# Performance work log

Measured on AMD Instinct MI355X. Metric: run time of the kernel, lower is better.

The kernel has to match this reference:

```python
import jax, jax.numpy as jnp
import numpy as np

D = 128      # d_model
H = 4        # n_heads
DH = D // H  # 32 head dim
TD = int(DH * 0.25)  # 8 time dims per head
T_DIM = TD * H       # 32 model-level time dims (MinkowskiLayerNorm t_dim)
EPS = 1e-5


def _ln(v, g, b):
    mu = jnp.mean(v, axis=-1, keepdims=True)
    var = jnp.mean(jnp.square(v - mu), axis=-1, keepdims=True)
    return (v - mu) * jax.lax.rsqrt(var + EPS) * g + b


def _minkowski_ln(x, gt, bt, gs, bs):
    # Normalize time-like and space-like coordinate blocks separately.
    return jnp.concatenate([_ln(x[..., :T_DIM], gt, bt), _ln(x[..., T_DIM:], gs, bs)], axis=-1)


def _lorentz_attn(x, Wq, bq, Wk, bk, Wv, bv, Wo, bo):
    B, S, _ = x.shape
    split = lambda y: y.reshape(B, S, H, DH).transpose(0, 2, 1, 3)  # [B,H,S,DH]
    q = split(x @ Wq + bq)
    k = split(x @ Wk + bk)
    v = split(x @ Wv + bv)
    # Minkowski metric signature (-,...,-,+,...,+): first TD dims of each head are time-like.
    eta = jnp.concatenate([-jnp.ones((TD,), x.dtype), jnp.ones((DH - TD,), x.dtype)])
    logits = jnp.einsum('bhqd,bhkd->bhqk', q * eta, k) / np.float32(np.sqrt(DH))
    w = jax.nn.softmax(logits, axis=-1)  # [B,H,S,S]
    o = jnp.einsum('bhqk,bhkd->bhqd', w, v).transpose(0, 2, 1, 3).reshape(B, S, D)
    return o @ Wo + bo


def setup_inputs() -> dict:
    key = jax.random.key(0)
    ks = jax.random.split(key, 8)
    s = 0.02
    inp = {
        'x': jax.random.normal(ks[0], (8, 2048, D), jnp.float32),
        'Wq': jax.random.normal(ks[1], (D, D), jnp.float32) * s,
        'bq': jnp.zeros((D,), jnp.float32),
        'Wk': jax.random.normal(ks[2], (D, D), jnp.float32) * s,
        'bk': jnp.zeros((D,), jnp.float32),
        'Wv': jax.random.normal(ks[3], (D, D), jnp.float32) * s,
        'bv': jnp.zeros((D,), jnp.float32),
        'Wo': jax.random.normal(ks[4], (D, D), jnp.float32) * s,
        'bo': jnp.zeros((D,), jnp.float32),
        'g1t': jnp.ones((T_DIM,), jnp.float32), 'b1t': jnp.zeros((T_DIM,), jnp.float32),
        'g1s': jnp.ones((D - T_DIM,), jnp.float32), 'b1s': jnp.zeros((D - T_DIM,), jnp.float32),
        'W1': jax.random.normal(ks[5], (D, 4 * D), jnp.float32) * s,
        'bf1': jnp.zeros((4 * D,), jnp.float32),
        'W2': jax.random.normal(ks[6], (4 * D, D), jnp.float32) * s,
        'bf2': jnp.zeros((D,), jnp.float32),
        'g2t': jnp.ones((T_DIM,), jnp.float32), 'b2t': jnp.zeros((T_DIM,), jnp.float32),
        'g2s': jnp.ones((D - T_DIM,), jnp.float32), 'b2s': jnp.zeros((D - T_DIM,), jnp.float32),
    }
    return inp


def reference(x, Wq, bq, Wk, bk, Wv, bv, Wo, bo,
              g1t, b1t, g1s, b1s, W1, bf1, W2, bf2,
              g2t, b2t, g2s, b2s):
    a = _lorentz_attn(x, Wq, bq, Wk, bk, Wv, bv, Wo, bo)
    x = _minkowski_ln(x + a, g1t, b1t, g1s, b1s)
    h = jax.nn.gelu(x @ W1 + bf1, approximate=False) @ W2 + bf2  # exact GELU (torch default)
    return _minkowski_ln(x + h, g2t, b2t, g2s, b2s)
```

## Files before the change

### kernel.cpp

```cpp
#include <hip/hip_runtime.h>
#include <hip/hip_bf16.h>

#define DEV __device__ __forceinline__

typedef __attribute__((ext_vector_type(8))) short short8;
typedef __attribute__((ext_vector_type(4))) float f32x4;

constexpr int D   = 128;
constexpr int S   = 2048;
constexpr int Hh  = 4;
constexpr int DH  = 32;
constexpr float QSCALE = 0.17677669529663687f * 1.4426950408889634f;
constexpr float EPSV = 1e-5f;

DEV unsigned short f2b(float f) {
  __hip_bfloat16 h = __float2bfloat16(f);
  return *reinterpret_cast<unsigned short*>(&h);
}
DEV unsigned pack2(float a, float b) {
  unsigned r;
  asm("v_cvt_pk_bf16_f32 %0, %1, %2" : "=v"(r) : "v"(a), "v"(b));
  return r;
}

DEV float fast_gelu(float v) {
  float z = v * 0.70710678118654752f;
  float a = fabsf(z);
  float t = __builtin_amdgcn_rcpf(1.0f + 0.3275911f * a);
  float p = t * (0.254829592f + t * (-0.284496736f +
            t * (1.421413741f + t * (-1.453152027f + t * 1.061405429f))));
  float e = __builtin_amdgcn_exp2f(-1.4426950408889634f * (z * z));
  float er = copysignf(1.0f - p * e, z);
  return 0.5f * v * (1.0f + er);
}


__global__ __launch_bounds__(256) void prep_kernel(
    const float* __restrict__ x,
    const float* __restrict__ Wq, const float* __restrict__ Wk,
    const float* __restrict__ Wv, const float* __restrict__ Wo,
    const float* __restrict__ W1, const float* __restrict__ W2,
    unsigned short* __restrict__ xb,
    unsigned short* __restrict__ wqT, unsigned short* __restrict__ wkT,
    unsigned short* __restrict__ wvT, unsigned short* __restrict__ woT,
    unsigned short* __restrict__ w1T, unsigned short* __restrict__ w2T) {
  int b = blockIdx.x, t = threadIdx.x;
  if (b < 1024) {
    int i8 = (b * 256 + t) * 8;
    int row = i8 >> 7, k0 = i8 & 127;
    const float4* p = reinterpret_cast<const float4*>(x + i8);
    float4 v0 = p[0], v1 = p[1];
    uint4 o;
    o.x = pack2(v0.x, v0.y);
    o.y = pack2(v0.z, v0.w);
    o.z = pack2(v1.x, v1.y);
    o.w = pack2(v1.z, v1.w);
    size_t off = ((size_t)(row >> 4) * 4 + (k0 >> 5)) * 512 + ((k0 & 31) >> 3) * 128 + (row & 15) * 8;
    *reinterpret_cast<uint4*>(xb + off) = o;
    return;
  }
  const float* src; unsigned short* dst; int K, N, base;
  if      (b < 1088) { src = Wq; dst = wqT; K = 128; N = 128; base = 1024; }
  else if (b < 1152) { src = Wk; dst = wkT; K = 128; N = 128; base = 1088; }
  else if (b < 1216) { src = Wv; dst = wvT; K = 128; N = 128; base = 1152; }
  else if (b < 1280) { src = Wo; dst = woT; K = 128; N = 128; base = 1216; }
  else if (b < 1536) { src = W1; dst = w1T; K = 128; N = 512; base = 1280; }
  else               { src = W2; dst = w2T; K = 512; N = 128; base = 1536; }
  int idx = (b - base) * 256 + t;
  int k = idx / N, n = idx - k * N;
  size_t off = ((size_t)(n >> 4) * (K >> 5) + (k >> 5)) * 512 + ((k & 31) >> 3) * 128 + (n & 15) * 8 + (k & 7);
  dst[off] = f2b(src[idx]);
}

template <int KDIM, bool SWAP>
DEV void gemm_tile_fl(const unsigned short* __restrict__ A,
                      const unsigned short* __restrict__ BT,
                      int tileA, int tileB0, int lane, f32x4 acc[8]) {
  constexpr int KS = KDIM / 32;
#pragma unroll
  for (int ks = 0; ks < KS; ++ks) {
    short8 a = *reinterpret_cast<const short8*>(A + ((size_t)(tileA * KS + ks) * 64 + lane) * 8);
#pragma unroll
    for (int c = 0; c < 8; ++c) {
      short8 b = *reinterpret_cast<const short8*>(BT + ((size_t)((tileB0 + c) * KS + ks) * 64 + lane) * 8);
      if constexpr (SWAP)
        acc[c] = __builtin_amdgcn_mfma_f32_16x16x32_bf16(b, a, acc[c], 0, 0, 0);
      else
        acc[c] = __builtin_amdgcn_mfma_f32_16x16x32_bf16(a, b, acc[c], 0, 0, 0);
    }
  }
}

__global__ __launch_bounds__(256) void qkv_kernel(
    const unsigned short* __restrict__ xb,
    const unsigned short* __restrict__ wqT, const unsigned short* __restrict__ wkT,
    const unsigned short* __restrict__ wvT,
    const float* __restrict__ bq, const float* __restrict__ bk, const float* __restrict__ bv,
    unsigned short* __restrict__ q, unsigned short* __restrict__ k,
    unsigned short* __restrict__ vT) {
  int w = threadIdx.x >> 6, lane = threadIdx.x & 63;
  int g = lane >> 4, ln = lane & 15;
  int z = blockIdx.y;
  int row0 = blockIdx.x * 64 + w * 16;
  int tileA = blockIdx.x * 4 + w;
  const unsigned short* BT = (z == 0) ? wqT : (z == 1) ? wkT : wvT;
  const float* bias = (z == 0) ? bq : (z == 1) ? bk : bv;
  f32x4 acc[8];
#pragma unroll
  for (int c = 0; c < 8; ++c) acc[c] = f32x4{0.f, 0.f, 0.f, 0.f};
  if (z == 2) {
    gemm_tile_fl<128, false>(xb, BT, tileA, 0, lane, acc);
    int t0 = row0 + 4 * g;
    int b_ = t0 >> 11, s0 = t0 & 2047;
#pragma unroll
    for (int c = 0; c < 8; ++c) {
      int n = c * 16 + ln;
      int h = n >> 5, dh = n & 31;
      float bi = bias[n];
      size_t tile = ((size_t)(b_ * Hh + h) * 32 + (s0 >> 6)) * 4 + ((s0 & 63) >> 5) * 2 + (dh >> 4);
      size_t off = tile * 512 + ((s0 & 31) >> 3) * 128 + (dh & 15) * 8 + (s0 & 7);
      uint2 st;
      st.x = pack2(acc[c][0] + bi, acc[c][1] + bi);
      st.y = pack2(acc[c][2] + bi, acc[c][3] + bi);
      *reinterpret_cast<uint2*>(vT + off) = st;
    }
  } else {
    gemm_tile_fl<128, true>(xb, BT, tileA, 0, lane, acc);
    unsigned short* dst = (z == 0) ? q : k;
    int t = row0 + ln;
    int b_ = t >> 11, s = t & 2047;
#pragma unroll
    for (int c = 0; c < 8; ++c) {
      int nc = c * 16 + 4 * g;
      int h = nc >> 5, dh0 = nc & 31;
      f32x4 bi = *reinterpret_cast<const f32x4*>(bias + nc);
      float f = 1.0f;
      if (z == 0) f = (dh0 < 8) ? -QSCALE : QSCALE;
      float v0 = (acc[c][0] + bi[0]) * f, v1 = (acc[c][1] + bi[1]) * f;
      float v2 = (acc[c][2] + bi[2]) * f, v3 = (acc[c][3] + bi[3]) * f;
      size_t tile = (size_t)(b_ * Hh + h) * 128 + (s >> 4);
      size_t off = tile * 512 + ((dh0 >> 3) * 16 + (s & 15)) * 8 + (dh0 & 7);
      uint2 st;
      st.x = pack2(v0, v1);
      st.y = pack2(v2, v3);
      *reinterpret_cast<uint2*>(dst + off) = st;
    }
  }
}

__global__ __launch_bounds__(512, 4) void attn_kernel(
    const unsigned short* __restrict__ q, const unsigned short* __restrict__ k,
    const unsigned short* __restrict__ vT, unsigned short* __restrict__ ao) {
  __shared__ float smem_f[7680];
  int w = threadIdx.x >> 6, lane = threadIdx.x & 63;
  int g = lane >> 4, ln = lane & 15;
  int w_q = w >> 2, w_kv = w & 3;
  int bh = blockIdx.y;
  int qbase = blockIdx.x * 64 + w_q * 32;
  const unsigned short* qp = q + (size_t)bh * S * DH + lane * 8;
  const unsigned short* kp = k + (size_t)bh * S * DH + lane * 8;
  const unsigned short* vp = vT + (size_t)bh * DH * S + lane * 8;

  short8 qfr[2];
#pragma unroll
  for (int qf = 0; qf < 2; ++qf)
    qfr[qf] = *reinterpret_cast<const short8*>(qp + (size_t)((qbase >> 4) + qf) * 512);

  short8 ones;
#pragma unroll
  for (int j = 0; j < 8; ++j) ones[j] = (short)0x3F80;

  float m[2] = {0.f, 0.f};
  int mz[2] = {1, 1};
  f32x4 acc[2][2];
  f32x4 acc_l[2];
#pragma unroll
  for (int a = 0; a < 2; ++a) {
    acc_l[a] = f32x4{0.f, 0.f, 0.f, 0.f};
#pragma unroll
    for (int b = 0; b < 2; ++b) acc[a][b] = f32x4{0.f, 0.f, 0.f, 0.f};
  }

  short8 kf[4];
  {
    int kv0 = w_kv * 512;
#pragma unroll
    for (int c = 0; c < 4; ++c)
      kf[c] = *reinterpret_cast<const short8*>(kp + (size_t)((kv0 >> 4) + c) * 512);
  }

#pragma unroll 2
  for (int kt = 0; kt < 8; ++kt) {
    int kv0 = w_kv * 512 + kt * 64;
    short8 vfr[2][2];
#pragma unroll
    for (int hv = 0; hv < 2; ++hv)
#pragma unroll
      for (int vf = 0; vf < 2; ++vf)
        vfr[hv][vf] = *reinterpret_cast<const short8*>(vp + (size_t)((kv0 >> 6) * 4 + hv * 2 + vf) * 512);
    short8 kf_n[4];
    {
      int ktn = (kt < 7) ? kt + 1 : 7;
      int kvn = w_kv * 512 + ktn * 64;
#pragma unroll
      for (int c = 0; c < 4; ++c)
        kf_n[c] = *reinterpret_cast<const short8*>(kp + (size_t)((kvn >> 4) + c) * 512);
    }
    f32x4 sst[4][2];
#pragma unroll
    for (int c = 0; c < 4; ++c)
#pragma unroll
      for (int qf = 0; qf < 2; ++qf)
        sst[c][qf] = __builtin_amdgcn_mfma_f32_16x16x32_bf16(kf[c], qfr[qf],
                                                             f32x4{0.f, 0.f, 0.f, 0.f}, 0, 0, 0);
    short8 pfr[2][2];
#pragma unroll
    for (int qf = 0; qf < 2; ++qf) {
      if (__builtin_amdgcn_readfirstlane(mz[qf])) {
#pragma unroll
        for (int c = 0; c < 4; ++c)
#pragma unroll
          for (int r = 0; r < 4; ++r)
            sst[c][qf][r] = __builtin_amdgcn_exp2f(sst[c][qf][r]);
      } else {
#pragma unroll
        for (int c = 0; c < 4; ++c)
#pragma unroll
          for (int r = 0; r < 4; ++r)
            sst[c][qf][r] = __builtin_amdgcn_exp2f(sst[c][qf][r] - m[qf]);
      }
      unsigned Wc[4][2];
#pragma unroll
      for (int c = 0; c < 4; ++c) {
        Wc[c][0] = pack2(sst[c][qf][0], sst[c][qf][1]);
        Wc[c][1] = pack2(sst[c][qf][2], sst[c][qf][3]);
      }
#pragma unroll
      for (int hv = 0; hv < 2; ++hv) {
        unsigned f00, f01, f10, f11;
        {
          auto st = __builtin_amdgcn_permlane32_swap(Wc[2 * hv][0], Wc[2 * hv + 1][0], false, false);
          auto uv = __builtin_amdgcn_permlane16_swap(st[0], st[1], false, false);
          f00 = uv[0]; f10 = uv[1];
        }
        {
          auto st = __builtin_amdgcn_permlane32_swap(Wc[2 * hv][1], Wc[2 * hv + 1][1], false, false);
          auto uv = __builtin_amdgcn_permlane16_swap(st[0], st[1], false, false);
          f01 = uv[0]; f11 = uv[1];
        }
        union { unsigned u[4]; short8 s8; } pu;
        pu.u[0] = f00; pu.u[1] = f01; pu.u[2] = f10; pu.u[3] = f11;
        pfr[qf][hv] = pu.s8;
      }
    }
    __builtin_amdgcn_s_setprio(1);
#pragma unroll
    for (int hv = 0; hv < 2; ++hv) {
#pragma unroll
      for (int qf = 0; qf < 2; ++qf) {
#pragma unroll
        for (int vf = 0; vf < 2; ++vf)
          acc[vf][qf] = __builtin_amdgcn_mfma_f32_16x16x32_bf16(vfr[hv][vf], pfr[qf][hv], acc[vf][qf], 0, 0, 0);
        acc_l[qf] = __builtin_amdgcn_mfma_f32_16x16x32_bf16(ones, pfr[qf][hv], acc_l[qf], 0, 0, 0);
      }
    }
    __builtin_amdgcn_s_setprio(0);
#pragma unroll
    for (int qf = 0; qf < 2; ++qf) {
      float ls = acc_l[qf][0];
      if (!__all(ls <= 16777216.0f)) {
        float lg = __builtin_amdgcn_logf(ls);
        float cs = __builtin_amdgcn_rcpf(ls);
        m[qf] += lg;
        mz[qf] = 0;
#pragma unroll
        for (int vf = 0; vf < 2; ++vf)
#pragma unroll
          for (int r = 0; r < 4; ++r) acc[vf][qf][r] *= cs;
#pragma unroll
        for (int r = 0; r < 4; ++r) acc_l[qf][r] *= cs;
      }
    }
#pragma unroll
    for (int c = 0; c < 4; ++c) kf[c] = kf_n[c];
  }
  __syncthreads();
  if (w_kv) {
    float* mb = smem_f + ((w_q * 3 + (w_kv - 1)) * 64 + lane) * 20;
    mb[0] = m[0]; mb[1] = m[1]; mb[2] = acc_l[0][0]; mb[3] = acc_l[1][0];
#pragma unroll
    for (int vf = 0; vf < 2; ++vf)
#pragma unroll
      for (int qf = 0; qf < 2; ++qf)
#pragma unroll
        for (int r = 0; r < 4; ++r) mb[4 + (vf * 2 + qf) * 4 + r] = acc[vf][qf][r];
  }
  __syncthreads();
  if (w_kv == 0) {
    const float* mb0 = smem_f + ((w_q * 3 + 0) * 64 + lane) * 20;
    const float* mb1 = smem_f + ((w_q * 3 + 1) * 64 + lane) * 20;
    const float* mb2 = smem_f + ((w_q * 3 + 2) * 64 + lane) * 20;
    int b_ = bh >> 2, h = bh & 3;
#pragma unroll
    for (int qf = 0; qf < 2; ++qf) {
      float mt = fmaxf(fmaxf(m[qf], mb0[qf]), fmaxf(mb1[qf], mb2[qf]));
      float e0 = __builtin_amdgcn_exp2f(m[qf] - mt);
      float e1 = __builtin_amdgcn_exp2f(mb0[qf] - mt);
      float e2 = __builtin_amdgcn_exp2f(mb1[qf] - mt);
      float e3 = __builtin_amdgcn_exp2f(mb2[qf] - mt);
      float lt = acc_l[qf][0] * e0 + mb0[2 + qf] * e1 + mb1[2 + qf] * e2 + mb2[2 + qf] * e3;
      float inv = 1.0f / lt;
      int qrow = qbase + qf * 16 + ln;
#pragma unroll
      for (int vf = 0; vf < 2; ++vf) {
        int kk = h * 32 + vf * 16 + 4 * g;
        float o[4];
        int ai = 4 + (vf * 2 + qf) * 4;
#pragma unroll
        for (int r = 0; r < 4; ++r)
          o[r] = (acc[vf][qf][r] * e0 + mb0[ai + r] * e1 + mb1[ai + r] * e2 + mb2[ai + r] * e3) * inv;
        uint2 st;
        st.x = pack2(o[0], o[1]);
        st.y = pack2(o[2], o[3]);
        size_t grow = (size_t)b_ * S + qrow;
        size_t off = ((grow >> 4) * 4 + (kk >> 5)) * 512 + ((kk & 31) >> 3) * 128 + (grow & 15) * 8 + (kk & 7);
        *reinterpret_cast<uint2*>(ao + off) = st;
      }
    }
  }
}

__global__ __launch_bounds__(256) void tail_kernel(
    const unsigned short* __restrict__ ao, const unsigned short* __restrict__ woT,
    const float* __restrict__ bo, const float* __restrict__ x,
    const float* __restrict__ g1t, const float* __restrict__ b1t,
    const float* __restrict__ g1s, const float* __restrict__ b1s,
    const unsigned short* __restrict__ w1T, const float* __restrict__ bf1,
    const unsigned short* __restrict__ w2T, const float* __restrict__ bf2,
    const float* __restrict__ g2t, const float* __restrict__ b2t,
    const float* __restrict__ g2s, const float* __restrict__ b2s,
    float* __restrict__ out) {
  __shared__ unsigned short xbl[16][136];
  __shared__ unsigned short hl[16][520];
  __shared__ float stats[4][16][2];
  int wn = threadIdx.x >> 6, lane = threadIdx.x & 63;
  int g = lane >> 4, ln = lane & 15;
  int row = blockIdx.x * 16 + ln;

  f32x4 acc1[2];
  acc1[0] = f32x4{0.f, 0.f, 0.f, 0.f};
  acc1[1] = f32x4{0.f, 0.f, 0.f, 0.f};
#pragma unroll
  for (int ks = 0; ks < 4; ++ks) {
    short8 a = *reinterpret_cast<const short8*>(ao + ((size_t)(blockIdx.x * 4 + ks) * 64 + lane) * 8);
#pragma unroll
    for (int c2 = 0; c2 < 2; ++c2) {
      short8 b = *reinterpret_cast<const short8*>(woT + ((size_t)((wn * 2 + c2) * 4 + ks) * 64 + lane) * 8);
      acc1[c2] = __builtin_amdgcn_mfma_f32_16x16x32_bf16(b, a, acc1[c2], 0, 0, 0);
    }
  }
  float rv[2][4];
  {
    float sum = 0.f, sq = 0.f;
#pragma unroll
    for (int c2 = 0; c2 < 2; ++c2) {
      int nc = wn * 32 + c2 * 16 + 4 * g;
      f32x4 bi = *reinterpret_cast<const f32x4*>(bo + nc);
      f32x4 xr = *reinterpret_cast<const f32x4*>(x + (size_t)row * D + nc);
#pragma unroll
      for (int r = 0; r < 4; ++r) {
        float v = acc1[c2][r] + bi[r] + xr[r];
        rv[c2][r] = v;
        sum += v; sq += v * v;
      }
    }
    sum += __shfl_xor(sum, 16); sum += __shfl_xor(sum, 32);
    sq  += __shfl_xor(sq, 16);  sq  += __shfl_xor(sq, 32);
    stats[wn][ln][0] = sum;
    stats[wn][ln][1] = sq;
  }
  __syncthreads();
  f32x4 xv[2];
  {
    float mu, rs;
    if (wn == 0) {
      float s = stats[0][ln][0], q2 = stats[0][ln][1];
      mu = s * (1.f / 32.f);
      rs = rsqrtf(q2 * (1.f / 32.f) - mu * mu + EPSV);
    } else {
      float s  = stats[1][ln][0] + stats[2][ln][0] + stats[3][ln][0];
      float q2 = stats[1][ln][1] + stats[2][ln][1] + stats[3][ln][1];
      mu = s * (1.f / 96.f);
      rs = rsqrtf(q2 * (1.f / 96.f) - mu * mu + EPSV);
    }
#pragma unroll
    for (int c2 = 0; c2 < 2; ++c2) {
      int nc = wn * 32 + c2 * 16 + 4 * g;
      f32x4 ga, bb;
      if (wn == 0) { ga = *reinterpret_cast<const f32x4*>(g1t + nc);
                     bb = *reinterpret_cast<const f32x4*>(b1t + nc); }
      else         { ga = *reinterpret_cast<const f32x4*>(g1s + nc - 32);
                     bb = *reinterpret_cast<const f32x4*>(b1s + nc - 32); }
#pragma unroll
      for (int r = 0; r < 4; ++r)
        xv[c2][r] = (rv[c2][r] - mu) * rs * ga[r] + bb[r];
      uint2 sb;
      sb.x = pack2(xv[c2][0], xv[c2][1]);
      sb.y = pack2(xv[c2][2], xv[c2][3]);
      *reinterpret_cast<uint2*>(&xbl[ln][nc]) = sb;
    }
  }
  __syncthreads();

  {
    f32x4 acc2[8];
#pragma unroll
    for (int c = 0; c < 8; ++c) acc2[c] = f32x4{0.f, 0.f, 0.f, 0.f};
#pragma unroll
    for (int ks = 0; ks < 4; ++ks) {
      short8 a = *reinterpret_cast<const short8*>(&xbl[ln][ks * 32 + 8 * g]);
#pragma unroll
      for (int c = 0; c < 8; ++c) {
        short8 b = *reinterpret_cast<const short8*>(w1T + ((size_t)((wn * 8 + c) * 4 + ks) * 64 + lane) * 8);
        acc2[c] = __builtin_amdgcn_mfma_f32_16x16x32_bf16(b, a, acc2[c], 0, 0, 0);
      }
    }
#pragma unroll
    for (int c = 0; c < 8; ++c) {
      int nc = wn * 128 + c * 16 + 4 * g;
      f32x4 bi = *reinterpret_cast<const f32x4*>(bf1 + nc);
      float ge[4];
#pragma unroll
      for (int r = 0; r < 4; ++r)
        ge[r] = fast_gelu(acc2[c][r] + bi[r]);
      uint2 stv;
      stv.x = pack2(ge[0], ge[1]);
      stv.y = pack2(ge[2], ge[3]);
      *reinterpret_cast<uint2*>(&hl[ln][nc]) = stv;
    }
  }
  __syncthreads();

  f32x4 acc3[2];
  acc3[0] = f32x4{0.f, 0.f, 0.f, 0.f};
  acc3[1] = f32x4{0.f, 0.f, 0.f, 0.f};
#pragma unroll
  for (int ks = 0; ks < 16; ++ks) {
    short8 a = *reinterpret_cast<const short8*>(&hl[ln][ks * 32 + 8 * g]);
#pragma unroll
    for (int c2 = 0; c2 < 2; ++c2) {
      short8 b = *reinterpret_cast<const short8*>(w2T + ((size_t)((wn * 2 + c2) * 16 + ks) * 64 + lane) * 8);
      acc3[c2] = __builtin_amdgcn_mfma_f32_16x16x32_bf16(b, a, acc3[c2], 0, 0, 0);
    }
  }
  float rv2[2][4];
  {
    float sum = 0.f, sq = 0.f;
#pragma unroll
    for (int c2 = 0; c2 < 2; ++c2) {
      int nc = wn * 32 + c2 * 16 + 4 * g;
      f32x4 bi = *reinterpret_cast<const f32x4*>(bf2 + nc);
#pragma unroll
      for (int r = 0; r < 4; ++r) {
        float v = acc3[c2][r] + bi[r] + xv[c2][r];
        rv2[c2][r] = v;
        sum += v; sq += v * v;
      }
    }
    sum += __shfl_xor(sum, 16); sum += __shfl_xor(sum, 32);
    sq  += __shfl_xor(sq, 16);  sq  += __shfl_xor(sq, 32);
    stats[wn][ln][0] = sum;
    stats[wn][ln][1] = sq;
  }
  __syncthreads();
  {
    float mu, rs;
    if (wn == 0) {
      float s = stats[0][ln][0], q2 = stats[0][ln][1];
      mu = s * (1.f / 32.f);
      rs = rsqrtf(q2 * (1.f / 32.f) - mu * mu + EPSV);
    } else {
      float s  = stats[1][ln][0] + stats[2][ln][0] + stats[3][ln][0];
      float q2 = stats[1][ln][1] + stats[2][ln][1] + stats[3][ln][1];
      mu = s * (1.f / 96.f);
      rs = rsqrtf(q2 * (1.f / 96.f) - mu * mu + EPSV);
    }
#pragma unroll
    for (int c2 = 0; c2 < 2; ++c2) {
      int nc = wn * 32 + c2 * 16 + 4 * g;
      f32x4 ga, bb;
      if (wn == 0) { ga = *reinterpret_cast<const f32x4*>(g2t + nc);
                     bb = *reinterpret_cast<const f32x4*>(b2t + nc); }
      else         { ga = *reinterpret_cast<const f32x4*>(g2s + nc - 32);
                     bb = *reinterpret_cast<const f32x4*>(b2s + nc - 32); }
      f32x4 o4;
#pragma unroll
      for (int r = 0; r < 4; ++r)
        o4[r] = (rv2[c2][r] - mu) * rs * ga[r] + bb[r];
      *reinterpret_cast<f32x4*>(out + (size_t)row * D + nc) = o4;
    }
  }
}

extern "C" void kernel_launch(void* const* d_in, const int* in_sizes, int n_in,
                              void* d_out, int out_size, void* d_ws, size_t ws_size,
                              hipStream_t stream) {
  (void)in_sizes; (void)n_in; (void)out_size; (void)ws_size;
  const float* x   = (const float*)d_in[0];
  const float* Wq  = (const float*)d_in[1];
  const float* bq  = (const float*)d_in[2];
  const float* Wk  = (const float*)d_in[3];
  const float* bk  = (const float*)d_in[4];
  const float* Wv  = (const float*)d_in[5];
  const float* bv  = (const float*)d_in[6];
  const float* Wo  = (const float*)d_in[7];
  const float* bo  = (const float*)d_in[8];
  const float* g1t = (const float*)d_in[9];
  const float* b1t = (const float*)d_in[10];
  const float* g1s = (const float*)d_in[11];
  const float* b1s = (const float*)d_in[12];
  const float* W1  = (const float*)d_in[13];
  const float* bf1 = (const float*)d_in[14];
  const float* W2  = (const float*)d_in[15];
  const float* bf2 = (const float*)d_in[16];
  const float* g2t = (const float*)d_in[17];
  const float* b2t = (const float*)d_in[18];
  const float* g2s = (const float*)d_in[19];
  const float* b2s = (const float*)d_in[20];

  char* ws = (char*)d_ws;
  unsigned short* xb  = (unsigned short*)(ws);
  unsigned short* wqT = (unsigned short*)(ws + 4194304);
  unsigned short* wkT = wqT + 16384;
  unsigned short* wvT = wkT + 16384;
  unsigned short* woT = wvT + 16384;
  unsigned short* w1T = woT + 16384;
  unsigned short* w2T = w1T + 65536;
  unsigned short* qb  = w2T + 65536;
  unsigned short* kb  = qb + 2097152;
  unsigned short* vT  = kb + 2097152;
  unsigned short* ao  = vT + 2097152;
  float* outp = (float*)d_out;

  prep_kernel<<<1792, 256, 0, stream>>>(x, Wq, Wk, Wv, Wo, W1, W2,
                                        xb, wqT, wkT, wvT, woT, w1T, w2T);
  qkv_kernel<<<dim3(256, 3), 256, 0, stream>>>(xb, wqT, wkT, wvT, bq, bk, bv, qb, kb, vT);
  attn_kernel<<<dim3(32, 32), 512, 0, stream>>>(qb, kb, vT, ao);
  tail_kernel<<<1024, 256, 0, stream>>>(ao, woT, bo, x, g1t, b1t, g1s, b1s,
                                        w1T, bf1, w2T, bf2, g2t, b2t, g2s, b2s, outp);
}
```

Baseline: 64.09 us.

## Give each attention wave 64 query rows to reuse K/V loads across more queries

The attention block shrinks from 8 waves (2 query groups × 4 KV splits) to 4 waves, each wave handling all 64 query rows of the block in two passes of 32. Each K and V fragment loaded is therefore reused for twice as many queries, halving K/V global traffic per block. The cost is more accumulator registers per wave, a lower launch-bounds occupancy hint, a wider shared-memory merge layout, and removal of the loop unroll pragma. The prep kernel also swaps integer division for shifts in the weight transpose.

After: 64.95 us. No clear change (+1.3%).

```diff
diff --git a/kernel.cpp b/kernel.cpp
--- a/kernel.cpp
+++ b/kernel.cpp
@@ -59,16 +59,16 @@
     *reinterpret_cast<uint4*>(xb + off) = o;
     return;
   }
-  const float* src; unsigned short* dst; int K, N, base;
-  if      (b < 1088) { src = Wq; dst = wqT; K = 128; N = 128; base = 1024; }
-  else if (b < 1152) { src = Wk; dst = wkT; K = 128; N = 128; base = 1088; }
-  else if (b < 1216) { src = Wv; dst = wvT; K = 128; N = 128; base = 1152; }
-  else if (b < 1280) { src = Wo; dst = woT; K = 128; N = 128; base = 1216; }
-  else if (b < 1536) { src = W1; dst = w1T; K = 128; N = 512; base = 1280; }
-  else               { src = W2; dst = w2T; K = 512; N = 128; base = 1536; }
+  const float* src; unsigned short* dst; int nsh, KS, base;
+  if      (b < 1088) { src = Wq; dst = wqT; nsh = 7; KS = 4;  base = 1024; }
+  else if (b < 1152) { src = Wk; dst = wkT; nsh = 7; KS = 4;  base = 1088; }
+  else if (b < 1216) { src = Wv; dst = wvT; nsh = 7; KS = 4;  base = 1152; }
+  else if (b < 1280) { src = Wo; dst = woT; nsh = 7; KS = 4;  base = 1216; }
+  else if (b < 1536) { src = W1; dst = w1T; nsh = 9; KS = 4;  base = 1280; }
+  else               { src = W2; dst = w2T; nsh = 7; KS = 16; base = 1536; }
   int idx = (b - base) * 256 + t;
-  int k = idx / N, n = idx - k * N;
-  size_t off = ((size_t)(n >> 4) * (K >> 5) + (k >> 5)) * 512 + ((k & 31) >> 3) * 128 + (n & 15) * 8 + (k & 7);
+  int k = idx >> nsh, n = idx & ((1 << nsh) - 1);
+  size_t off = ((size_t)(n >> 4) * KS + (k >> 5)) * 512 + ((k & 31) >> 3) * 128 + (n & 15) * 8 + (k & 7);
   dst[off] = f2b(src[idx]);
 }
 
@@ -148,37 +148,36 @@
   }
 }
 
-__global__ __launch_bounds__(512, 4) void attn_kernel(
+__global__ __launch_bounds__(256, 2) void attn_kernel(
     const unsigned short* __restrict__ q, const unsigned short* __restrict__ k,
     const unsigned short* __restrict__ vT, unsigned short* __restrict__ ao) {
   __shared__ float smem_f[7680];
-  int w = threadIdx.x >> 6, lane = threadIdx.x & 63;
+  int w_kv = threadIdx.x >> 6, lane = threadIdx.x & 63;
   int g = lane >> 4, ln = lane & 15;
-  int w_q = w >> 2, w_kv = w & 3;
   int bh = blockIdx.y;
-  int qbase = blockIdx.x * 64 + w_q * 32;
+  int qbase = blockIdx.x * 64;
   const unsigned short* qp = q + (size_t)bh * S * DH + lane * 8;
   const unsigned short* kp = k + (size_t)bh * S * DH + lane * 8;
   const unsigned short* vp = vT + (size_t)bh * DH * S + lane * 8;
 
-  short8 qfr[2];
-#pragma unroll
-  for (int qf = 0; qf < 2; ++qf)
+  short8 qfr[4];
+#pragma unroll
+  for (int qf = 0; qf < 4; ++qf)
     qfr[qf] = *reinterpret_cast<const short8*>(qp + (size_t)((qbase >> 4) + qf) * 512);
 
   short8 ones;
 #pragma unroll
   for (int j = 0; j < 8; ++j) ones[j] = (short)0x3F80;
 
-  float m[2] = {0.f, 0.f};
-  int mz[2] = {1, 1};
-  f32x4 acc[2][2];
-  f32x4 acc_l[2];
-#pragma unroll
-  for (int a = 0; a < 2; ++a) {
+  float m[4] = {0.f, 0.f, 0.f, 0.f};
+  int mz[4] = {1, 1, 1, 1};
+  f32x4 acc[2][4];
+  f32x4 acc_l[4];
+#pragma unroll
+  for (int a = 0; a < 4; ++a) {
     acc_l[a] = f32x4{0.f, 0.f, 0.f, 0.f};
 #pragma unroll
-    for (int b = 0; b < 2; ++b) acc[a][b] = f32x4{0.f, 0.f, 0.f, 0.f};
+    for (int b = 0; b < 2; ++b) acc[b][a] = f32x4{0.f, 0.f, 0.f, 0.f};
   }
 
   short8 kf[4];
@@ -189,7 +188,6 @@
       kf[c] = *reinterpret_cast<const short8*>(kp + (size_t)((kv0 >> 4) + c) * 512);
   }
 
-#pragma unroll 2
   for (int kt = 0; kt < 8; ++kt) {
     int kv0 = w_kv * 512 + kt * 64;
     short8 vfr[2][2];
@@ -206,79 +204,84 @@
       for (int c = 0; c < 4; ++c)
         kf_n[c] = *reinterpret_cast<const short8*>(kp + (size_t)((kvn >> 4) + c) * 512);
     }
-    f32x4 sst[4][2];
-#pragma unroll
-    for (int c = 0; c < 4; ++c)
-#pragma unroll
-      for (int qf = 0; qf < 2; ++qf)
-        sst[c][qf] = __builtin_amdgcn_mfma_f32_16x16x32_bf16(kf[c], qfr[qf],
-                                                             f32x4{0.f, 0.f, 0.f, 0.f}, 0, 0, 0);
-    short8 pfr[2][2];
-#pragma unroll
-    for (int qf = 0; qf < 2; ++qf) {
-      if (__builtin_amdgcn_readfirstlane(mz[qf])) {
-#pragma unroll
-        for (int c = 0; c < 4; ++c)
-#pragma unroll
-          for (int r = 0; r < 4; ++r)
-            sst[c][qf][r] = __builtin_amdgcn_exp2f(sst[c][qf][r]);
-      } else {
-#pragma unroll
-        for (int c = 0; c < 4; ++c)
-#pragma unroll
-          for (int r = 0; r < 4; ++r)
-            sst[c][qf][r] = __builtin_amdgcn_exp2f(sst[c][qf][r] - m[qf]);
-      }
-      unsigned Wc[4][2];
-#pragma unroll
-      for (int c = 0; c < 4; ++c) {
-        Wc[c][0] = pack2(sst[c][qf][0], sst[c][qf][1]);
-        Wc[c][1] = pack2(sst[c][qf][2], sst[c][qf][3]);
-      }
+#pragma unroll
+    for (int p = 0; p < 2; ++p) {
+      f32x4 sst[4][2];
+#pragma unroll
+      for (int c = 0; c < 4; ++c)
+#pragma unroll
+        for (int j = 0; j < 2; ++j)
+          sst[c][j] = __builtin_amdgcn_mfma_f32_16x16x32_bf16(kf[c], qfr[2 * p + j],
+                                                              f32x4{0.f, 0.f, 0.f, 0.f}, 0, 0, 0);
+      short8 pfr[2][2];
+#pragma unroll
+      for (int j = 0; j < 2; ++j) {
+        int qf = 2 * p + j;
+        if (__builtin_amdgcn_readfirstlane(mz[qf])) {
+#pragma unroll
+          for (int c = 0; c < 4; ++c)
+#pragma unroll
+            for (int r = 0; r < 4; ++r)
+              sst[c][j][r] = __builtin_amdgcn_exp2f(sst[c][j][r]);
+        } else {
+#pragma unroll
+          for (int c = 0; c < 4; ++c)
+#pragma unroll
+            for (int r = 0; r < 4; ++r)
+              sst[c][j][r] = __builtin_amdgcn_exp2f(sst[c][j][r] - m[qf]);
+        }
+        unsigned Wc[4][2];
+#pragma unroll
+        for (int c = 0; c < 4; ++c) {
+          Wc[c][0] = pack2(sst[c][j][0], sst[c][j][1]);
+          Wc[c][1] = pack2(sst[c][j][2], sst[c][j][3]);
+        }
+#pragma unroll
+        for (int hv = 0; hv < 2; ++hv) {
+          unsigned f00, f01, f10, f11;
+          {
+            auto st = __builtin_amdgcn_permlane32_swap(Wc[2 * hv][0], Wc[2 * hv + 1][0], false, false);
+            auto uv = __builtin_amdgcn_permlane16_swap(st[0], st[1], false, false);
+            f00 = uv[0]; f10 = uv[1];
+          }
+          {
+            auto st = __builtin_amdgcn_permlane32_swap(Wc[2 * hv][1], Wc[2 * hv + 1][1], false, false);
+            auto uv = __builtin_amdgcn_permlane16_swap(st[0], st[1], false, false);
+            f01 = uv[0]; f11 = uv[1];
+          }
+          union { unsigned u[4]; short8 s8; } pu;
+          pu.u[0] = f00; pu.u[1] = f01; pu.u[2] = f10; pu.u[3] = f11;
+          pfr[j][hv] = pu.s8;
+        }
+      }
+      __builtin_amdgcn_s_setprio(1);
 #pragma unroll
       for (int hv = 0; hv < 2; ++hv) {
-        unsigned f00, f01, f10, f11;
-        {
-          auto st = __builtin_amdgcn_permlane32_swap(Wc[2 * hv][0], Wc[2 * hv + 1][0], false, false);
-          auto uv = __builtin_amdgcn_permlane16_swap(st[0], st[1], false, false);
-          f00 = uv[0]; f10 = uv[1];
+#pragma unroll
+        for (int j = 0; j < 2; ++j) {
+#pragma unroll
+          for (int vf = 0; vf < 2; ++vf)
+            acc[vf][2 * p + j] = __builtin_amdgcn_mfma_f32_16x16x32_bf16(vfr[hv][vf], pfr[j][hv], acc[vf][2 * p + j], 0, 0, 0);
+          acc_l[2 * p + j] = __builtin_amdgcn_mfma_f32_16x16x32_bf16(ones, pfr[j][hv], acc_l[2 * p + j], 0, 0, 0);
         }
-        {
-          auto st = __builtin_amdgcn_permlane32_swap(Wc[2 * hv][1], Wc[2 * hv + 1][1], false, false);
-          auto uv = __builtin_amdgcn_permlane16_swap(st[0], st[1], false, false);
-          f01 = uv[0]; f11 = uv[1];
+      }
+      __builtin_amdgcn_s_setprio(0);
+#pragma unroll
+      for (int j = 0; j < 2; ++j) {
+        int qf = 2 * p + j;
+        float ls = acc_l[qf][0];
+        if (!__all(ls <= 16777216.0f)) {
+          float lg = __builtin_amdgcn_logf(ls);
+          float cs = __builtin_amdgcn_rcpf(ls);
+          m[qf] += lg;
+          mz[qf] = 0;
+#pragma unroll
+          for (int vf = 0; vf < 2; ++vf)
+#pragma unroll
+            for (int r = 0; r < 4; ++r) acc[vf][qf][r] *= cs;
+#pragma unroll
+          for (int r = 0; r < 4; ++r) acc_l[qf][r] *= cs;
         }
-        union { unsigned u[4]; short8 s8; } pu;
-        pu.u[0] = f00; pu.u[1] = f01; pu.u[2] = f10; pu.u[3] = f11;
-        pfr[qf][hv] = pu.s8;
-      }
-    }
-    __builtin_amdgcn_s_setprio(1);
-#pragma unroll
-    for (int hv = 0; hv < 2; ++hv) {
-#pragma unroll
-      for (int qf = 0; qf < 2; ++qf) {
-#pragma unroll
-        for (int vf = 0; vf < 2; ++vf)
-          acc[vf][qf] = __builtin_amdgcn_mfma_f32_16x16x32_bf16(vfr[hv][vf], pfr[qf][hv], acc[vf][qf], 0, 0, 0);
-        acc_l[qf] = __builtin_amdgcn_mfma_f32_16x16x32_bf16(ones, pfr[qf][hv], acc_l[qf], 0, 0, 0);
-      }
-    }
-    __builtin_amdgcn_s_setprio(0);
-#pragma unroll
-    for (int qf = 0; qf < 2; ++qf) {
-      float ls = acc_l[qf][0];
-      if (!__all(ls <= 16777216.0f)) {
-        float lg = __builtin_amdgcn_logf(ls);
-        float cs = __builtin_amdgcn_rcpf(ls);
-        m[qf] += lg;
-        mz[qf] = 0;
-#pragma unroll
-        for (int vf = 0; vf < 2; ++vf)
-#pragma unroll
-          for (int r = 0; r < 4; ++r) acc[vf][qf][r] *= cs;
-#pragma unroll
-        for (int r = 0; r < 4; ++r) acc_l[qf][r] *= cs;
       }
     }
 #pragma unroll
@@ -286,36 +289,37 @@
   }
   __syncthreads();
   if (w_kv) {
-    float* mb = smem_f + ((w_q * 3 + (w_kv - 1)) * 64 + lane) * 20;
-    mb[0] = m[0]; mb[1] = m[1]; mb[2] = acc_l[0][0]; mb[3] = acc_l[1][0];
+    float* mb = smem_f + ((w_kv - 1) * 64 + lane) * 40;
+#pragma unroll
+    for (int qf = 0; qf < 4; ++qf) { mb[qf] = m[qf]; mb[4 + qf] = acc_l[qf][0]; }
 #pragma unroll
     for (int vf = 0; vf < 2; ++vf)
 #pragma unroll
-      for (int qf = 0; qf < 2; ++qf)
-#pragma unroll
-        for (int r = 0; r < 4; ++r) mb[4 + (vf * 2 + qf) * 4 + r] = acc[vf][qf][r];
+      for (int qf = 0; qf < 4; ++qf)
+#pragma unroll
+        for (int r = 0; r < 4; ++r) mb[8 + (vf * 4 + qf) * 4 + r] = acc[vf][qf][r];
   }
   __syncthreads();
   if (w_kv == 0) {
-    const float* mb0 = smem_f + ((w_q * 3 + 0) * 64 + lane) * 20;
-    const float* mb1 = smem_f + ((w_q * 3 + 1) * 64 + lane) * 20;
-    const float* mb2 = smem_f + ((w_q * 3 + 2) * 64 + lane) * 20;
+    const float* mb0 = smem_f + (0 * 64 + lane) * 40;
+    const float* mb1 = smem_f + (1 * 64 + lane) * 40;
+    const float* mb2 = smem_f + (2 * 64 + lane) * 40;
     int b_ = bh >> 2, h = bh & 3;
 #pragma unroll
-    for (int qf = 0; qf < 2; ++qf) {
+    for (int qf = 0; qf < 4; ++qf) {
       float mt = fmaxf(fmaxf(m[qf], mb0[qf]), fmaxf(mb1[qf], mb2[qf]));
       float e0 = __builtin_amdgcn_exp2f(m[qf] - mt);
       float e1 = __builtin_amdgcn_exp2f(mb0[qf] - mt);
       float e2 = __builtin_amdgcn_exp2f(mb1[qf] - mt);
       float e3 = __builtin_amdgcn_exp2f(mb2[qf] - mt);
-      float lt = acc_l[qf][0] * e0 + mb0[2 + qf] * e1 + mb1[2 + qf] * e2 + mb2[2 + qf] * e3;
+      float lt = acc_l[qf][0] * e0 + mb0[4 + qf] * e1 + mb1[4 + qf] * e2 + mb2[4 + qf] * e3;
       float inv = 1.0f / lt;
       int qrow = qbase + qf * 16 + ln;
 #pragma unroll
       for (int vf = 0; vf < 2; ++vf) {
         int kk = h * 32 + vf * 16 + 4 * g;
+        int ai = 8 + (vf * 4 + qf) * 4;
         float o[4];
-        int ai = 4 + (vf * 2 + qf) * 4;
 #pragma unroll
         for (int r = 0; r < 4; ++r)
           o[r] = (acc[vf][qf][r] * e0 + mb0[ai + r] * e1 + mb1[ai + r] * e2 + mb2[ai + r] * e3) * inv;
@@ -545,7 +549,7 @@
   prep_kernel<<<1792, 256, 0, stream>>>(x, Wq, Wk, Wv, Wo, W1, W2,
                                         xb, wqT, wkT, wvT, woT, w1T, w2T);
   qkv_kernel<<<dim3(256, 3), 256, 0, stream>>>(xb, wqT, wkT, wvT, bq, bk, bv, qb, kb, vT);
-  attn_kernel<<<dim3(32, 32), 512, 0, stream>>>(qb, kb, vT, ao);
+  attn_kernel<<<dim3(32, 32), 256, 0, stream>>>(qb, kb, vT, ao);
   tail_kernel<<<1024, 256, 0, stream>>>(ao, woT, bo, x, g1t, b1t, g1s, b1s,
                                         w1T, bf1, w2T, bf2, g2t, b2t, g2s, b2s, outp);
 }
```
